# Optimization experiments

Hardware: AMD Instinct MI355X
Metric: run time of the kernel (lower is better)

The kernel has to match this reference:

```python
import jax, jax.numpy as jnp
import numpy as np

N_NODES = 100000
N_EDGES = 6400000
N_GRAPHS = 1000
D_IN = 16
D_HID = 16
D_OUT = 6


def setup_inputs() -> dict:
    key = jax.random.key(0)
    ks = jax.random.split(key, 12)
    x = jax.random.normal(ks[0], (N_NODES, D_IN), dtype=jnp.float32)
    edge_index = jax.random.randint(ks[1], (2, N_EDGES), 0, N_NODES, dtype=jnp.int64)
    edge_attr = jax.random.normal(ks[2], (N_EDGES, D_IN), dtype=jnp.float32)
    batch = jnp.sort(jax.random.randint(ks[3], (N_NODES,), 0, N_GRAPHS, dtype=jnp.int64))
    s = 1.0 / np.sqrt(D_HID)
    W1a = jax.random.uniform(ks[4], (D_IN, D_HID), jnp.float32, -s, s)
    b1a = jax.random.uniform(ks[5], (D_HID,), jnp.float32, -s, s)
    W1b = jax.random.uniform(ks[6], (D_HID, D_HID), jnp.float32, -s, s)
    b1b = jax.random.uniform(ks[7], (D_HID,), jnp.float32, -s, s)
    W2a = jax.random.uniform(ks[8], (D_HID, D_OUT), jnp.float32, -s, s)
    b2a = jax.random.uniform(ks[9], (D_OUT,), jnp.float32, -s, s)
    W2b = jax.random.uniform(ks[10], (D_OUT, D_OUT), jnp.float32, -s, s)
    b2b = jax.random.uniform(ks[11], (D_OUT,), jnp.float32, -s, s)
    return {"x": x, "edge_index": edge_index, "edge_attr": edge_attr, "batch": batch,
            "W1a": W1a, "b1a": b1a, "W1b": W1b, "b1b": b1b,
            "W2a": W2a, "b2a": b2a, "W2b": W2b, "b2b": b2b}


def _gine_conv(x, edge_index, edge_attr, mlp):
    # message: relu(x_j + e), aggregated by sum at target node; eps = 0
    src, dst = edge_index[0], edge_index[1]
    msg = jax.nn.relu(x[src] + edge_attr)                       # [E, D]
    aggr = jax.ops.segment_sum(msg, dst, num_segments=N_NODES)  # [N, D]
    return mlp(x + aggr)


def reference(x, edge_index, edge_attr, batch,
              W1a, b1a, W1b, b1b, W2a, b2a, W2b, b2b):
    mlp1 = lambda h: jax.nn.relu(h @ W1a + b1a) @ W1b + b1b
    mlp2 = lambda h: jax.nn.relu(h @ W2a + b2a) @ W2b + b2b
    h = _gine_conv(x, edge_index, edge_attr, mlp1)
    h = jax.nn.relu(h)  # dropout is identity in eval mode
    h = _gine_conv(h, edge_index, edge_attr, mlp2)
    # global mean pool over graphs
    sums = jax.ops.segment_sum(h, batch, num_segments=N_GRAPHS)          # [G, D_OUT]
    counts = jax.ops.segment_sum(jnp.ones((N_NODES,), h.dtype), batch,
                                 num_segments=N_GRAPHS)
    pooled = sums / jnp.maximum(counts, 1.0)[:, None]
    return jax.nn.log_softmax(pooled, axis=1)
```

## Files before the change

### kernel.cpp

```cpp
#include <hip/hip_runtime.h>
#include <math.h>

#define N_NODES  100000
#define N_EDGES  6400000
#define N_GRAPHS 1000
#define D_IN  16
#define D_HID 16
#define D_OUT 6

#define B_NODES   64
#define NBUCK     ((N_NODES + B_NODES - 1) / B_NODES)
#define CAPB      4608
#define NSLOTS    ((size_t)NBUCK * CAPB)
#define EPB       16384
#define KBLOCKS   ((N_EDGES + EPB - 1) / EPB)

__global__ __launch_bounds__(1024) void scatter_direct(
    const int* __restrict__ ei, int* __restrict__ cnt, int2* __restrict__ tmp)
{
    __shared__ int hist[NBUCK];
    __shared__ int base[NBUCK];
    int t = threadIdx.x;
    for (int i = t; i < NBUCK; i += 1024) hist[i] = 0;
    __syncthreads();
    int e0 = blockIdx.x * EPB;
#pragma unroll
    for (int k = 0; k < EPB / 1024; ++k) {
        int e = e0 + k * 1024 + t;
        if (e < N_EDGES) atomicAdd(&hist[ei[N_EDGES + e] >> 6], 1);
    }
    __syncthreads();
    for (int i = t; i < NBUCK; i += 1024) {
        int h = hist[i];
        base[i] = h ? atomicAdd(&cnt[i], h) : 0;
        hist[i] = 0;
    }
    __syncthreads();
#pragma unroll
    for (int k = 0; k < EPB / 1024; ++k) {
        int e = e0 + k * 1024 + t;
        if (e < N_EDGES) {
            int dst = ei[N_EDGES + e];
            int src = ei[e];
            int b = dst >> 6;
            int r = base[b] + atomicAdd(&hist[b], 1);
            if (r < CAPB)
                tmp[(size_t)b * CAPB + r] = make_int2(((dst & 63) << 23) | e, src);
        }
    }
}

__global__ __launch_bounds__(1024) void bucket_place(
    const int* __restrict__ cnt, const int2* __restrict__ tmp,
    int2* __restrict__ csr, int2* __restrict__ offs2)
{
    __shared__ int2 stage[CAPB];
    __shared__ int hist[B_NODES];
    int b = blockIdx.x, t = threadIdx.x;
    int m = cnt[b];
    if (m > CAPB) m = CAPB;
    int beg = b * CAPB;
    for (int i = t; i < m; i += 1024) stage[i] = tmp[beg + i];
    if (t < B_NODES) hist[t] = 0;
    __syncthreads();
    for (int i = t; i < m; i += 1024)
        atomicAdd(&hist[(stage[i].x >> 23) & 63], 1);
    __syncthreads();
    if (t < 64) {
        int v = hist[t], sc = v;
#pragma unroll
        for (int d = 1; d < 64; d <<= 1) {
            int o = __shfl_up(sc, d, 64);
            if (t >= d) sc += o;
        }
        int ex = sc - v;
        int node = b * 64 + t;
        if (node < N_NODES) offs2[node] = make_int2(beg + ex, beg + ex + v);
        hist[t] = ex;
    }
    __syncthreads();
    for (int i = t; i < m; i += 1024) {
        int2 p = stage[i];
        int d = (p.x >> 23) & 63;
        int e = p.x & 0x7FFFFF;
        int r = atomicAdd(&hist[d], 1);
        csr[beg + r] = make_int2(p.y, e);
    }
}

__global__ __launch_bounds__(256) void gather_csr(
    const int2* __restrict__ offs2, const int2* __restrict__ csr,
    const float* __restrict__ feat, const float* __restrict__ eattr,
    float* __restrict__ aggr)
{
    int t = threadIdx.x;
    int lane = t & 15, grp = t >> 4;
    int n = blockIdx.x * 16 + grp;
    if (n >= N_NODES) return;
    int2 oo = offs2[n];
    int i = oo.x, end = oo.y;
    float acc = 0.0f;
    for (; i + 8 <= end; i += 8) {
        int2 p[8];
#pragma unroll
        for (int k = 0; k < 8; ++k) p[k] = csr[i + k];
        float ev[8];
#pragma unroll
        for (int k = 0; k < 8; ++k)
            ev[k] = __builtin_nontemporal_load(eattr + (size_t)p[k].y * 16 + lane);
        float fv[8];
#pragma unroll
        for (int k = 0; k < 8; ++k)
            fv[k] = feat[(size_t)p[k].x * 16 + lane];
#pragma unroll
        for (int k = 0; k < 8; ++k)
            acc += fmaxf(ev[k] + fv[k], 0.0f);
    }
    for (; i < end; ++i) {
        int2 p = csr[i];
        acc += fmaxf(__builtin_nontemporal_load(eattr + (size_t)p.y * 16 + lane)
                     + feat[(size_t)p.x * 16 + lane], 0.0f);
    }
    aggr[(size_t)n * 16 + lane] = acc;
}

__global__ __launch_bounds__(256) void node1_kernel(
    const float* __restrict__ x, const float* __restrict__ aggr,
    const float* __restrict__ W1a, const float* __restrict__ b1a,
    const float* __restrict__ W1b, const float* __restrict__ b1b,
    float* __restrict__ h)
{
    __shared__ float sWa[256], sWb[256], sba[16], sbb[16];
    int t = threadIdx.x;
    if (t < 256) { sWa[t] = W1a[t]; sWb[t] = W1b[t]; }
    if (t < 16)  { sba[t] = b1a[t]; sbb[t] = b1b[t]; }
    __syncthreads();

    int n = blockIdx.x * blockDim.x + t;
    if (n >= N_NODES) return;

    float v[16];
#pragma unroll
    for (int i = 0; i < 16; ++i) v[i] = x[n * 16 + i] + aggr[n * 16 + i];

    float u[16];
#pragma unroll
    for (int j = 0; j < 16; ++j) {
        float s = sba[j];
#pragma unroll
        for (int i = 0; i < 16; ++i) s += v[i] * sWa[i * 16 + j];
        u[j] = fmaxf(s, 0.0f);
    }
#pragma unroll
    for (int j = 0; j < 16; ++j) {
        float s = sbb[j];
#pragma unroll
        for (int i = 0; i < 16; ++i) s += u[i] * sWb[i * 16 + j];
        h[n * 16 + j] = fmaxf(s, 0.0f);
    }
}

__global__ __launch_bounds__(256) void node2_kernel(
    const float* __restrict__ h, const float* __restrict__ aggr,
    const int* __restrict__ batch,
    const float* __restrict__ W2a, const float* __restrict__ b2a,
    const float* __restrict__ W2b, const float* __restrict__ b2b,
    float* __restrict__ sums, float* __restrict__ counts)
{
    __shared__ float sWa[16 * 6], sWb[6 * 6], sba[6], sbb[6];
    int t = threadIdx.x;
    if (t < 96) sWa[t] = W2a[t];
    if (t < 36) sWb[t] = W2b[t];
    if (t < 6)  { sba[t] = b2a[t]; sbb[t] = b2b[t]; }
    __syncthreads();

    int n = blockIdx.x * blockDim.x + t;
    if (n >= N_NODES) return;

    float v[16];
#pragma unroll
    for (int i = 0; i < 16; ++i) v[i] = h[n * 16 + i] + aggr[n * 16 + i];

    float u[6];
#pragma unroll
    for (int j = 0; j < 6; ++j) {
        float s = sba[j];
#pragma unroll
        for (int i = 0; i < 16; ++i) s += v[i] * sWa[i * 6 + j];
        u[j] = fmaxf(s, 0.0f);
    }
    int g = batch[n];
#pragma unroll
    for (int j = 0; j < 6; ++j) {
        float s = sbb[j];
#pragma unroll
        for (int i = 0; i < 6; ++i) s += u[i] * sWb[i * 6 + j];
        atomicAdd(&sums[g * 6 + j], s);
    }
    atomicAdd(&counts[g], 1.0f);
}

__global__ __launch_bounds__(256) void pool_kernel(
    const float* __restrict__ sums, const float* __restrict__ counts,
    float* __restrict__ out)
{
    int g = blockIdx.x * blockDim.x + threadIdx.x;
    if (g >= N_GRAPHS) return;
    float c = fmaxf(counts[g], 1.0f);
    float p[6];
    float mx = -INFINITY;
#pragma unroll
    for (int j = 0; j < 6; ++j) {
        p[j] = sums[g * 6 + j] / c;
        mx = fmaxf(mx, p[j]);
    }
    float se = 0.0f;
#pragma unroll
    for (int j = 0; j < 6; ++j) se += expf(p[j] - mx);
    float lse = mx + logf(se);
#pragma unroll
    for (int j = 0; j < 6; ++j) out[g * 6 + j] = p[j] - lse;
}

extern "C" void kernel_launch(void* const* d_in, const int* in_sizes, int n_in,
                              void* d_out, int out_size, void* d_ws, size_t ws_size,
                              hipStream_t stream)
{
    const float* x     = (const float*)d_in[0];
    const int*   ei    = (const int*)  d_in[1];
    const float* eattr = (const float*)d_in[2];
    const int*   batch = (const int*)  d_in[3];
    const float* W1a = (const float*)d_in[4];
    const float* b1a = (const float*)d_in[5];
    const float* W1b = (const float*)d_in[6];
    const float* b1b = (const float*)d_in[7];
    const float* W2a = (const float*)d_in[8];
    const float* b2a = (const float*)d_in[9];
    const float* W2b = (const float*)d_in[10];
    const float* b2b = (const float*)d_in[11];
    float* out = (float*)d_out;

    int2*  tmp    = (int2*)d_ws;
    int2*  csr    = tmp + NSLOTS;
    float* aggr   = (float*)(csr + NSLOTS);
    float* h      = aggr + (size_t)N_NODES * 16;
    int2*  offs2  = (int2*)(h + (size_t)N_NODES * 16);
    int*   cnt    = (int*)(offs2 + N_NODES);
    float* sums   = (float*)(cnt + NBUCK);
    float* counts = sums + (size_t)N_GRAPHS * 6;

    const int TB = 256;
    const int node_blocks = (N_NODES + TB - 1) / TB;
    const int gather_blocks = (N_NODES + 15) / 16;

    hipMemsetAsync(cnt, 0, (size_t)NBUCK * sizeof(int), stream);
    scatter_direct<<<KBLOCKS, 1024, 0, stream>>>(ei, cnt, tmp);
    bucket_place<<<NBUCK, 1024, 0, stream>>>(cnt, tmp, csr, offs2);

    gather_csr<<<gather_blocks, TB, 0, stream>>>(offs2, csr, x, eattr, aggr);
    node1_kernel<<<node_blocks, TB, 0, stream>>>(x, aggr, W1a, b1a, W1b, b1b, h);

    gather_csr<<<gather_blocks, TB, 0, stream>>>(offs2, csr, h, eattr, aggr);
    hipMemsetAsync(sums, 0, (size_t)(N_GRAPHS * 6 + N_GRAPHS) * sizeof(float), stream);
    node2_kernel<<<node_blocks, TB, 0, stream>>>(h, aggr, batch, W2a, b2a, W2b, b2b,
                                                 sums, counts);

    pool_kernel<<<(N_GRAPHS + TB - 1) / TB, TB, 0, stream>>>(sums, counts, out);
}
```

Baseline: 639.0 us.

## Stash edge attributes as CSR-ordered bf16 during first gather for second layer

The first aggregation pass now also writes each edge's attribute row, rounded to bf16, into a buffer laid out in CSR order. The second aggregation reads this compact, contiguous copy with 8 lanes per node and float2 feature loads, instead of randomly gathering the fp32 edge_attr rows again. The aim is to cut the second layer's attribute traffic in half and make it coalesced. The cost is extra write traffic in the first pass, a larger workspace, and bf16 rounding error in the second layer's messages.

```diff
diff --git a/kernel.cpp b/kernel.cpp
--- a/kernel.cpp
+++ b/kernel.cpp
@@ -88,10 +88,10 @@
     }
 }
 
-__global__ __launch_bounds__(256) void gather_csr(
+__global__ __launch_bounds__(256) void gather_stage(
     const int2* __restrict__ offs2, const int2* __restrict__ csr,
     const float* __restrict__ feat, const float* __restrict__ eattr,
-    float* __restrict__ aggr)
+    float* __restrict__ aggr, unsigned short* __restrict__ attrb)
 {
     int t = threadIdx.x;
     int lane = t & 15, grp = t >> 4;
@@ -113,15 +113,65 @@
         for (int k = 0; k < 8; ++k)
             fv[k] = feat[(size_t)p[k].x * 16 + lane];
 #pragma unroll
-        for (int k = 0; k < 8; ++k)
+        for (int k = 0; k < 8; ++k) {
+            unsigned bits = __float_as_uint(ev[k]);
+            attrb[(size_t)(i + k) * 16 + lane] =
+                (unsigned short)((bits + 0x7FFFu + ((bits >> 16) & 1u)) >> 16);
             acc += fmaxf(ev[k] + fv[k], 0.0f);
+        }
     }
     for (; i < end; ++i) {
         int2 p = csr[i];
-        acc += fmaxf(__builtin_nontemporal_load(eattr + (size_t)p.y * 16 + lane)
-                     + feat[(size_t)p.x * 16 + lane], 0.0f);
+        float e4 = __builtin_nontemporal_load(eattr + (size_t)p.y * 16 + lane);
+        unsigned bits = __float_as_uint(e4);
+        attrb[(size_t)i * 16 + lane] =
+            (unsigned short)((bits + 0x7FFFu + ((bits >> 16) & 1u)) >> 16);
+        acc += fmaxf(e4 + feat[(size_t)p.x * 16 + lane], 0.0f);
     }
     aggr[(size_t)n * 16 + lane] = acc;
+}
+
+__global__ void gather_lin(
+    const int2* __restrict__ offs2, const int2* __restrict__ csr,
+    const float* __restrict__ feat, const unsigned short* __restrict__ attrb,
+    float* __restrict__ aggr)
+{
+    int t = threadIdx.x;
+    int lane = t & 7, grp = t >> 3;
+    int n = blockIdx.x * 32 + grp;
+    if (n >= N_NODES) return;
+    int2 oo = offs2[n];
+    int i = oo.x, end = oo.y;
+    const unsigned* attr32 = (const unsigned*)attrb;
+    float accx = 0.0f, accy = 0.0f;
+    for (; i + 8 <= end; i += 8) {
+        int s[8];
+#pragma unroll
+        for (int k = 0; k < 8; ++k) s[k] = csr[i + k].x;
+        unsigned a[8];
+#pragma unroll
+        for (int k = 0; k < 8; ++k)
+            a[k] = attr32[(size_t)(i + k) * 8 + lane];
+        float2 f[8];
+#pragma unroll
+        for (int k = 0; k < 8; ++k)
+            f[k] = *(const float2*)(feat + (size_t)s[k] * 16 + lane * 2);
+#pragma unroll
+        for (int k = 0; k < 8; ++k) {
+            float a0 = __uint_as_float(a[k] << 16);
+            float a1 = __uint_as_float(a[k] & 0xFFFF0000u);
+            accx += fmaxf(a0 + f[k].x, 0.0f);
+            accy += fmaxf(a1 + f[k].y, 0.0f);
+        }
+    }
+    for (; i < end; ++i) {
+        int src = csr[i].x;
+        unsigned a = attr32[(size_t)i * 8 + lane];
+        float2 f = *(const float2*)(feat + (size_t)src * 16 + lane * 2);
+        accx += fmaxf(__uint_as_float(a << 16) + f.x, 0.0f);
+        accy += fmaxf(__uint_as_float(a & 0xFFFF0000u) + f.y, 0.0f);
+    }
+    *(float2*)(aggr + (size_t)n * 16 + lane * 2) = make_float2(accx, accy);
 }
 
 __global__ __launch_bounds__(256) void node1_kernel(
@@ -242,7 +292,8 @@
 
     int2*  tmp    = (int2*)d_ws;
     int2*  csr    = tmp + NSLOTS;
-    float* aggr   = (float*)(csr + NSLOTS);
+    unsigned short* attrb = (unsigned short*)(csr + NSLOTS);
+    float* aggr   = (float*)(attrb + NSLOTS * 16);
     float* h      = aggr + (size_t)N_NODES * 16;
     int2*  offs2  = (int2*)(h + (size_t)N_NODES * 16);
     int*   cnt    = (int*)(offs2 + N_NODES);
@@ -251,16 +302,17 @@
 
     const int TB = 256;
     const int node_blocks = (N_NODES + TB - 1) / TB;
-    const int gather_blocks = (N_NODES + 15) / 16;
+    const int g1_blocks = (N_NODES + 15) / 16;
+    const int g2_blocks = (N_NODES + 31) / 32;
 
     hipMemsetAsync(cnt, 0, (size_t)NBUCK * sizeof(int), stream);
     scatter_direct<<<KBLOCKS, 1024, 0, stream>>>(ei, cnt, tmp);
     bucket_place<<<NBUCK, 1024, 0, stream>>>(cnt, tmp, csr, offs2);
 
-    gather_csr<<<gather_blocks, TB, 0, stream>>>(offs2, csr, x, eattr, aggr);
+    gather_stage<<<g1_blocks, TB, 0, stream>>>(offs2, csr, x, eattr, aggr, attrb);
     node1_kernel<<<node_blocks, TB, 0, stream>>>(x, aggr, W1a, b1a, W1b, b1b, h);
 
-    gather_csr<<<gather_blocks, TB, 0, stream>>>(offs2, csr, h, eattr, aggr);
+    gather_lin<<<g2_blocks, TB, 0, stream>>>(offs2, csr, h, attrb, aggr);
     hipMemsetAsync(sums, 0, (size_t)(N_GRAPHS * 6 + N_GRAPHS) * sizeof(float), stream);
     node2_kernel<<<node_blocks, TB, 0, stream>>>(h, aggr, batch, W2a, b2a, W2b, b2b,
                                                  sums, counts);
```

After: 688.4 us. 7.7% more time.

## Fuse first-layer gather into bucket placement kernel

Applied to the files above, without the earlier changes.

Merges the bucket placement pass with the first edge gather so each bucket block, after building its CSR slice, immediately aggregates messages for its 64 nodes. This removes one kernel launch and lets the freshly written CSR entries be reread while likely still in cache. The trade-off is that each 1024-thread block handles 64 nodes with 16 lanes each, so the gather now runs under the large block's LDS footprint (4608 int2 stage) and lower occupancy than the separate 256-thread gather.

```diff
diff --git a/kernel.cpp b/kernel.cpp
--- a/kernel.cpp
+++ b/kernel.cpp
@@ -50,12 +50,15 @@
     }
 }
 
-__global__ __launch_bounds__(1024) void bucket_place(
+__global__ __launch_bounds__(1024) void place_gather(
     const int* __restrict__ cnt, const int2* __restrict__ tmp,
-    int2* __restrict__ csr, int2* __restrict__ offs2)
+    const float* __restrict__ feat, const float* __restrict__ eattr,
+    int2* __restrict__ csr, int2* __restrict__ offs2,
+    float* __restrict__ aggr)
 {
     __shared__ int2 stage[CAPB];
     __shared__ int hist[B_NODES];
+    __shared__ int nodebeg[B_NODES];
     int b = blockIdx.x, t = threadIdx.x;
     int m = cnt[b];
     if (m > CAPB) m = CAPB;
@@ -76,6 +79,7 @@
         int ex = sc - v;
         int node = b * 64 + t;
         if (node < N_NODES) offs2[node] = make_int2(beg + ex, beg + ex + v);
+        nodebeg[t] = ex;
         hist[t] = ex;
     }
     __syncthreads();
@@ -86,6 +90,36 @@
         int r = atomicAdd(&hist[d], 1);
         csr[beg + r] = make_int2(p.y, e);
     }
+    __syncthreads();
+
+    int lane = t & 15, grp = t >> 4;
+    int n = b * 64 + grp;
+    if (n >= N_NODES) return;
+    int i = beg + nodebeg[grp];
+    int end = beg + hist[grp];
+    float acc = 0.0f;
+    for (; i + 8 <= end; i += 8) {
+        int2 p[8];
+#pragma unroll
+        for (int k = 0; k < 8; ++k) p[k] = csr[i + k];
+        float ev[8];
+#pragma unroll
+        for (int k = 0; k < 8; ++k)
+            ev[k] = __builtin_nontemporal_load(eattr + (size_t)p[k].y * 16 + lane);
+        float fv[8];
+#pragma unroll
+        for (int k = 0; k < 8; ++k)
+            fv[k] = feat[(size_t)p[k].x * 16 + lane];
+#pragma unroll
+        for (int k = 0; k < 8; ++k)
+            acc += fmaxf(ev[k] + fv[k], 0.0f);
+    }
+    for (; i < end; ++i) {
+        int2 p = csr[i];
+        acc += fmaxf(__builtin_nontemporal_load(eattr + (size_t)p.y * 16 + lane)
+                     + feat[(size_t)p.x * 16 + lane], 0.0f);
+    }
+    aggr[(size_t)n * 16 + lane] = acc;
 }
 
 __global__ __launch_bounds__(256) void gather_csr(
@@ -251,16 +285,14 @@
 
     const int TB = 256;
     const int node_blocks = (N_NODES + TB - 1) / TB;
-    const int gather_blocks = (N_NODES + 15) / 16;
+    const int g2_blocks = (N_NODES + 15) / 16;
 
     hipMemsetAsync(cnt, 0, (size_t)NBUCK * sizeof(int), stream);
     scatter_direct<<<KBLOCKS, 1024, 0, stream>>>(ei, cnt, tmp);
-    bucket_place<<<NBUCK, 1024, 0, stream>>>(cnt, tmp, csr, offs2);
-
-    gather_csr<<<gather_blocks, TB, 0, stream>>>(offs2, csr, x, eattr, aggr);
+    place_gather<<<NBUCK, 1024, 0, stream>>>(cnt, tmp, x, eattr, csr, offs2, aggr);
     node1_kernel<<<node_blocks, TB, 0, stream>>>(x, aggr, W1a, b1a, W1b, b1b, h);
 
-    gather_csr<<<gather_blocks, TB, 0, stream>>>(offs2, csr, h, eattr, aggr);
+    gather_csr<<<g2_blocks, TB, 0, stream>>>(offs2, csr, h, eattr, aggr);
     hipMemsetAsync(sums, 0, (size_t)(N_GRAPHS * 6 + N_GRAPHS) * sizeof(float), stream);
     node2_kernel<<<node_blocks, TB, 0, stream>>>(h, aggr, batch, W2a, b2a, W2b, b2b,
                                                  sums, counts);
```

New measurement: 651.5 us. Within noise of the previous version (+1.9%).
